# Optimization experiments

Measured on AMD Instinct MI355X. Metric: run time of the kernel, lower is better.

The kernel has to match this reference:

```python
import jax, jax.numpy as jnp
import numpy as np

FILTER_LENGTH = 2048
HOP_LENGTH = 512
CUTOFF = FILTER_LENGTH // 2 + 1  # 1025


def _make_forward_basis():
    # Real/imag rows of DFT matrix, modulated by periodic Hann window.
    fourier_basis = np.fft.fft(np.eye(FILTER_LENGTH))
    basis = np.vstack([np.real(fourier_basis[:CUTOFF, :]),
                       np.imag(fourier_basis[:CUTOFF, :])])  # [2050, 2048]
    n = np.arange(FILTER_LENGTH)
    hann = 0.5 - 0.5 * np.cos(2.0 * np.pi * n / FILTER_LENGTH)  # fftbins=True
    basis = basis * hann[None, :]
    return jnp.asarray(basis[:, None, :], dtype=jnp.float32)  # [2050, 1, 2048]


def setup_inputs() -> dict:
    key = jax.random.key(0)
    input_data = jax.random.normal(key, (32, 320000), dtype=jnp.float32)
    forward_basis = _make_forward_basis()
    return {"input_data": input_data, "forward_basis": forward_basis}


def reference(input_data, forward_basis):
    B = input_data.shape[0]
    pad = FILTER_LENGTH // 2
    x = jnp.pad(input_data, ((0, 0), (pad, pad)), mode="reflect")  # [B, N+2048]
    x = x[:, None, :]  # [B, 1, T]
    ft = jax.lax.conv_general_dilated(
        x, forward_basis,
        window_strides=(HOP_LENGTH,),
        padding="VALID",
        dimension_numbers=("NCH", "OIH", "NCH"),
    )  # [B, 2050, frames]
    real = ft[:, :CUTOFF, :]
    imag = ft[:, CUTOFF:, :]
    return jnp.sqrt(real * real + imag * imag)
```

## Files before the change

kernel.cpp:

```cpp
#include <hip/hip_runtime.h>
#include <hip/hip_bf16.h>
#include <cstdint>


#define FILT   2048
#define HOP    512
#define CUT    1025
#define NBATCH 32
#define TFR    626
#define NFR    (NBATCH * TFR)
#define LSIG   320000
#define LPAD   (LSIG + FILT)
#define N2     1024
#define MWS    1088
#define KT     17
#define TT     20

typedef __attribute__((ext_vector_type(8))) short short8;

__device__ __forceinline__ short bf16r(float f) {
  __hip_bfloat16 h = __float2bfloat16(f);
  return __builtin_bit_cast(short, h);
}
__device__ __forceinline__ float bf2f(uint32_t u) {
  return __builtin_bit_cast(float, u << 16);
}

__device__ __forceinline__ short8 pack8(float4 a, float4 b) {
  short8 v;
  v[0] = bf16r(a.x); v[1] = bf16r(a.y); v[2] = bf16r(a.z); v[3] = bf16r(a.w);
  v[4] = bf16r(b.x); v[5] = bf16r(b.y); v[6] = bf16r(b.z); v[7] = bf16r(b.w);
  return v;
}

__global__ void pad_signal(const float* __restrict__ x, short* __restrict__ XP) {
  const int b = blockIdx.y;
  const int i0 = (blockIdx.x * 256 + threadIdx.x) * 8;
  if (i0 >= LPAD) return;
  const float* xb = x + (size_t)b * LSIG;
  const int j0 = i0 - 1024;
  short8 v;
  if (j0 >= 0 && j0 + 8 <= LSIG) {
    float4 a = *(const float4*)(xb + j0);
    float4 c = *(const float4*)(xb + j0 + 4);
    v = pack8(a, c);
  } else {
    #pragma unroll
    for (int e = 0; e < 8; ++e) {
      int j = j0 + e;
      j = j < 0 ? -j : (j >= LSIG ? 2 * LSIG - 2 - j : j);
      v[e] = bf16r(xb[j]);
    }
  }
  *(short8*)&XP[(size_t)b * LPAD + i0] = v;
}

__global__ void make_tables(float* __restrict__ hann, float2* __restrict__ Tst,
                            float2* __restrict__ Tun) {
  const int i = blockIdx.x * 256 + threadIdx.x;
  const float PI2 = 6.283185307179586f;
  if (i < 2048) hann[i] = 0.5f - 0.5f * cosf(PI2 * (float)i / 2048.0f);
  if (i < 1024) {
    float s, c;
    sincosf(-PI2 * (float)i / 1024.0f, &s, &c);
    Tst[i] = make_float2(c, s);
    sincosf(-PI2 * (float)i / 2048.0f, &s, &c);
    Tun[i] = make_float2(c, s);
  }
}

__device__ __forceinline__ float2 cmul(float2 a, float2 b) {
  return make_float2(a.x * b.x - a.y * b.y, a.x * b.y + a.y * b.x);
}
__device__ __forceinline__ float2 cmulc(float2 a, float cx, float cy) {
  return make_float2(a.x * cx - a.y * cy, a.x * cy + a.y * cx);
}

__device__ __forceinline__ int SW(int i) { return i ^ ((i >> 4) & 15); }

__device__ __forceinline__ void fft16(float2* y) {
  static constexpr float TX[4][4] = {
    {1.f, 1.f, 1.f, 1.f},
    {1.f,  0.92387953251128674f,  0.70710678118654752f,  0.38268343236508978f},
    {1.f,  0.70710678118654752f,  0.f,                  -0.70710678118654752f},
    {1.f,  0.38268343236508978f, -0.70710678118654752f, -0.92387953251128674f}};
  static constexpr float TY[4][4] = {
    {0.f, 0.f, 0.f, 0.f},
    {0.f, -0.38268343236508978f, -0.70710678118654752f, -0.92387953251128674f},
    {0.f, -0.70710678118654752f, -1.f,                  -0.70710678118654752f},
    {0.f, -0.92387953251128674f, -0.70710678118654752f,  0.38268343236508978f}};
  float2 G[16];
  #pragma unroll
  for (int n0 = 0; n0 < 4; ++n0) {
    float2 a0 = y[n0], a1 = y[n0 + 4], a2 = y[n0 + 8], a3 = y[n0 + 12];
    float2 e = make_float2(a0.x + a2.x, a0.y + a2.y);
    float2 f = make_float2(a0.x - a2.x, a0.y - a2.y);
    float2 g = make_float2(a1.x + a3.x, a1.y + a3.y);
    float2 h = make_float2(a1.x - a3.x, a1.y - a3.y);
    float2 F0 = make_float2(e.x + g.x, e.y + g.y);
    float2 F1 = make_float2(f.x + h.y, f.y - h.x);
    float2 F2 = make_float2(e.x - g.x, e.y - g.y);
    float2 F3 = make_float2(f.x - h.y, f.y + h.x);
    G[n0 * 4 + 0] = F0;
    G[n0 * 4 + 1] = cmulc(F1, TX[n0][1], TY[n0][1]);
    G[n0 * 4 + 2] = cmulc(F2, TX[n0][2], TY[n0][2]);
    G[n0 * 4 + 3] = cmulc(F3, TX[n0][3], TY[n0][3]);
  }
  #pragma unroll
  for (int q = 0; q < 4; ++q) {
    float2 a0 = G[q], a1 = G[4 + q], a2 = G[8 + q], a3 = G[12 + q];
    float2 e = make_float2(a0.x + a2.x, a0.y + a2.y);
    float2 f = make_float2(a0.x - a2.x, a0.y - a2.y);
    float2 g = make_float2(a1.x + a3.x, a1.y + a3.y);
    float2 h = make_float2(a1.x - a3.x, a1.y - a3.y);
    y[q]      = make_float2(e.x + g.x, e.y + g.y);
    y[q + 4]  = make_float2(f.x + h.y, f.y - h.x);
    y[q + 8]  = make_float2(e.x - g.x, e.y - g.y);
    y[q + 12] = make_float2(f.x - h.y, f.y + h.x);
  }
}

template<int LOG>
__device__ __forceinline__ void fft_stage(float2* z, const float2* tw, int lane) {
  constexpr int M4 = 1 << LOG;
  constexpr int STRIDE = 1 << (8 - LOG);
  #pragma unroll
  for (int u = 0; u < 4; ++u) {
    const int bf = u * 64 + lane;
    const int j  = bf & (M4 - 1);
    const int i0 = ((bf >> LOG) << (LOG + 2)) | j;
    const int i1 = i0 + M4, i2 = i0 + 2 * M4, i3 = i0 + 3 * M4;
    const int p0 = SW(i0), p1 = SW(i1), p2 = SW(i2), p3 = SW(i3);
    float2 a = z[p0], b = z[p1], c = z[p2], d = z[p3];
    if (LOG > 0) {
      b = cmul(b, tw[j * STRIDE]);
      c = cmul(c, tw[2 * j * STRIDE]);
      d = cmul(d, tw[3 * j * STRIDE]);
    }
    const float2 t0 = make_float2(a.x + c.x, a.y + c.y);
    const float2 t1 = make_float2(a.x - c.x, a.y - c.y);
    const float2 t2 = make_float2(b.x + d.x, b.y + d.y);
    const float2 t3 = make_float2(b.x - d.x, b.y - d.y);
    z[p0] = make_float2(t0.x + t2.x, t0.y + t2.y);
    z[p1] = make_float2(t1.x + t3.y, t1.y - t3.x);
    z[p2] = make_float2(t0.x - t2.x, t0.y - t2.y);
    z[p3] = make_float2(t1.x - t3.y, t1.y + t3.x);
  }
}

__global__ __launch_bounds__(256)
void stft_fft(const short* __restrict__ XP, const float* __restrict__ hann,
              const float2* __restrict__ Tst, const float2* __restrict__ Tun,
              ushort* __restrict__ MW)
{
  __shared__ float2 zsh[4][1024];
  __shared__ float2 tst[1024];

  const int tid = threadIdx.x, wv = tid >> 6, lane = tid & 63;
  #pragma unroll
  for (int u = 0; u < 4; ++u) tst[u * 256 + tid] = Tst[u * 256 + tid];
  __syncthreads();

  float2* z = zsh[wv];

  const int G  = ((lane & 3) << 4) | (lane & 12) | (lane >> 4);
  const int zb = 16 * G, gm = G & 15;

  const int f = blockIdx.x * 4 + wv;
  const int b = f / TFR, t = f - b * TFR;
  const short* base = XP + (size_t)b * LPAD + (size_t)t * HOP;

  float2 y[16];
  #pragma unroll
  for (int u = 0; u < 16; ++u) {
    const int n = u * 64 + lane;
    const uint32_t pr = *(const uint32_t*)(base + 2 * n);
    const float2 h = *(const float2*)(hann + 2 * n);
    y[u] = make_float2(bf2f(pr & 0xffffu) * h.x, bf2f(pr >> 16) * h.y);
  }
  fft16(y);
  #pragma unroll
  for (int k = 0; k < 16; ++k) z[zb + (k ^ gm)] = y[k];

  fft_stage<4>(z, tst, lane);
  fft_stage<6>(z, tst, lane);
  fft_stage<8>(z, tst, lane);

  ushort* mw = MW + (size_t)f * MWS;
  #pragma unroll
  for (int v = 0; v < 8; ++v) {
    const int k = v * 64 + lane;
    const float2 Zk = z[SW(k)];
    const int km = (N2 - k) & (N2 - 1);
    const float2 Zm = z[SW(km)];
    const float xer = 0.5f * (Zk.x + Zm.x);
    const float xei = 0.5f * (Zk.y - Zm.y);
    const float xor_ = 0.5f * (Zk.y + Zm.y);
    const float xoi = -0.5f * (Zk.x - Zm.x);
    const float2 w = Tun[k];
    const float px = w.x * xor_ - w.y * xoi;
    const float py = w.x * xoi + w.y * xor_;
    const float Xr = xer + px, Xi = xei + py;
    const float Yr = xer - px, Yi = xei - py;
    mw[k]        = (ushort)bf16r(sqrtf(Xr * Xr + Xi * Xi));
    mw[1024 - k] = (ushort)bf16r(sqrtf(Yr * Yr + Yi * Yi));
  }
  if (lane == 0) {
    const float2 Zc = z[SW(512)];
    mw[512] = (ushort)bf16r(sqrtf(Zc.x * Zc.x + Zc.y * Zc.y));
  }
}

__global__ __launch_bounds__(256)
void transpose_out(const ushort* __restrict__ MW, float* __restrict__ out) {
  __shared__ float tile[64][33];
  const int b  = blockIdx.y;
  const int kt = blockIdx.x % KT;
  const int tt = blockIdx.x / KT;
  const int k0 = kt * 64, t0 = tt * 32;
  const int tid = threadIdx.x;
  const int r = tid >> 5, c = tid & 31;

  #pragma unroll
  for (int s = 0; s < 4; ++s) {
    const int t = t0 + r + 8 * s;
    if (t < TFR) {
      const uint32_t pr =
        *(const uint32_t*)(MW + (size_t)(b * TFR + t) * MWS + k0 + 2 * c);
      tile[2 * c][r + 8 * s]     = bf2f(pr & 0xffffu);
      tile[2 * c + 1][r + 8 * s] = bf2f(pr >> 16);
    }
  }
  __syncthreads();

  const int kk = tid >> 2, toff = (tid & 3) * 8;
  const int k = k0 + kk;
  if (k < CUT) {
    float* pptr = out + (size_t)b * (CUT * TFR) + (size_t)k * TFR + t0 + toff;
    if (t0 + 32 <= TFR) {
      float4 v0 = make_float4(tile[kk][toff], tile[kk][toff + 1],
                              tile[kk][toff + 2], tile[kk][toff + 3]);
      float4 v1 = make_float4(tile[kk][toff + 4], tile[kk][toff + 5],
                              tile[kk][toff + 6], tile[kk][toff + 7]);
      *(float4*)pptr = v0;
      *(float4*)(pptr + 4) = v1;
    } else {
      #pragma unroll
      for (int e = 0; e < 8; ++e) {
        const int t = t0 + toff + e;
        if (t < TFR) pptr[e] = tile[kk][toff + e];
      }
    }
  }
}

typedef __attribute__((ext_vector_type(4))) float f32x4;

__global__ __launch_bounds__(256, 2)
void stft_gemm_fb(const float* __restrict__ basis, const float* __restrict__ x,
                  float* __restrict__ out)
{
  __shared__ alignas(16) short sA[2][128][64];
  __shared__ alignas(16) short sB[128][64];

  const int tid  = threadIdx.x;
  const int wave = tid >> 6;
  const int lane = tid & 63;
  const int n0 = blockIdx.x * 128;
  const int m0 = blockIdx.y * 128;

  f32x4 acc_r[4][4], acc_i[4][4];
  #pragma unroll
  for (int i = 0; i < 4; ++i)
    #pragma unroll
    for (int j = 0; j < 4; ++j) { acc_r[i][j] = (f32x4)0.f; acc_i[i][j] = (f32x4)0.f; }

  const int sr = tid >> 1;
  const int sh = (tid & 1) * 32;

  for (int k0 = 0; k0 < FILT; k0 += 64) {
    #pragma unroll
    for (int p = 0; p < 2; ++p) {
      const int k = m0 + sr;
      short8 v[4];
      if (k < CUT) {
        const float* src = basis + (size_t)(p * CUT + k) * FILT + k0 + sh;
        #pragma unroll
        for (int qq = 0; qq < 4; ++qq) {
          float4 a = *(const float4*)(src + qq * 8);
          float4 b = *(const float4*)(src + qq * 8 + 4);
          v[qq] = pack8(a, b);
        }
      } else {
        #pragma unroll
        for (int qq = 0; qq < 4; ++qq) v[qq] = (short8)(short)0;
      }
      #pragma unroll
      for (int qq = 0; qq < 4; ++qq) *(short8*)&sA[p][sr][sh + qq * 8] = v[qq];
    }
    {
      const int f = n0 + sr;
      short8 v[4];
      if (f < NFR) {
        const int b = f / TFR, t = f - b * TFR;
        const float* xb = x + (size_t)b * LSIG;
        const int j0 = t * HOP + k0 + sh - 1024;
        if (j0 >= 0 && j0 + 32 <= LSIG) {
          #pragma unroll
          for (int qq = 0; qq < 4; ++qq) {
            float4 a  = *(const float4*)(xb + j0 + qq * 8);
            float4 b2 = *(const float4*)(xb + j0 + qq * 8 + 4);
            v[qq] = pack8(a, b2);
          }
        } else {
          #pragma unroll
          for (int qq = 0; qq < 4; ++qq)
            #pragma unroll
            for (int e = 0; e < 8; ++e) {
              int j = j0 + qq * 8 + e;
              j = j < 0 ? -j : (j >= LSIG ? 2 * LSIG - 2 - j : j);
              v[qq][e] = bf16r(xb[j]);
            }
        }
      } else {
        #pragma unroll
        for (int qq = 0; qq < 4; ++qq) v[qq] = (short8)(short)0;
      }
      #pragma unroll
      for (int qq = 0; qq < 4; ++qq) *(short8*)&sB[sr][sh + qq * 8] = v[qq];
    }
    __syncthreads();

    const int ra = lane & 15;
    #pragma unroll
    for (int kk = 0; kk < 64; kk += 32) {
      const int col = kk + (lane >> 4) * 8;
      short8 arr[4], aii[4], bfr[4];
      #pragma unroll
      for (int i = 0; i < 4; ++i) {
        const int rm = (wave >> 1) * 64 + i * 16 + ra;
        arr[i] = *(const short8*)&sA[0][rm][col];
        aii[i] = *(const short8*)&sA[1][rm][col];
        const int rn = (wave & 1) * 64 + i * 16 + ra;
        bfr[i] = *(const short8*)&sB[rn][col];
      }
      #pragma unroll
      for (int i = 0; i < 4; ++i)
        #pragma unroll
        for (int j = 0; j < 4; ++j) {
          acc_r[i][j] = __builtin_amdgcn_mfma_f32_16x16x32_bf16(arr[i], bfr[j], acc_r[i][j], 0, 0, 0);
          acc_i[i][j] = __builtin_amdgcn_mfma_f32_16x16x32_bf16(aii[i], bfr[j], acc_i[i][j], 0, 0, 0);
        }
    }
    __syncthreads();
  }

  const int wm0 = m0 + (wave >> 1) * 64;
  const int wn0 = n0 + (wave & 1) * 64;
  const int cl = lane & 15;
  const int rg = (lane >> 4) * 4;
  #pragma unroll
  for (int j = 0; j < 4; ++j) {
    const int f = wn0 + j * 16 + cl;
    if (f >= NFR) continue;
    const int b = f / TFR, t = f - b * TFR;
    float* ob = out + (size_t)b * (CUT * TFR) + t;
    #pragma unroll
    for (int i = 0; i < 4; ++i) {
      #pragma unroll
      for (int r = 0; r < 4; ++r) {
        const int k = wm0 + i * 16 + rg + r;
        if (k < CUT) {
          float re = acc_r[i][j][r], im = acc_i[i][j][r];
          ob[(size_t)k * TFR] = sqrtf(re * re + im * im);
        }
      }
    }
  }
}

extern "C" void kernel_launch(void* const* d_in, const int* in_sizes, int n_in,
                              void* d_out, int out_size, void* d_ws, size_t ws_size,
                              hipStream_t stream) {
  const float* x     = (const float*)d_in[0];
  const float* basis = (const float*)d_in[1];
  float* out = (float*)d_out;

  const size_t sbytes = (size_t)NBATCH * LPAD * sizeof(short);
  const size_t hbytes = 2048 * sizeof(float);
  const size_t tbytes = 1024 * sizeof(float2);
  const size_t mbytes = (size_t)NFR * MWS * sizeof(ushort);

  if (ws_size >= sbytes + hbytes + 2 * tbytes + mbytes) {
    short*  XP   = (short*)d_ws;
    float*  hann = (float*)((char*)d_ws + sbytes);
    float2* Tst  = (float2*)((char*)d_ws + sbytes + hbytes);
    float2* Tun  = (float2*)((char*)d_ws + sbytes + hbytes + tbytes);
    ushort* MW   = (ushort*)((char*)d_ws + sbytes + hbytes + 2 * tbytes);
    pad_signal<<<dim3((LPAD + 2047) / 2048, NBATCH), 256, 0, stream>>>(x, XP);
    make_tables<<<8, 256, 0, stream>>>(hann, Tst, Tun);
    stft_fft<<<NFR / 4, 256, 0, stream>>>(XP, hann, Tst, Tun, MW);
    transpose_out<<<dim3(KT * TT, NBATCH), 256, 0, stream>>>(MW, out);
  } else {
    stft_gemm_fb<<<dim3(157, 9), 256, 0, stream>>>(basis, x, out);
  }
}
```

Baseline: 96.39 us.

## Fuse reflect padding into FFT kernel and merge two radix-4 stages in registers

Removes the separate pad_signal kernel that wrote a bf16 padded copy of the signal; the FFT kernel now reads fp32 input directly, handling reflect padding only for edge frames. It also merges the first two shared-memory radix-4 stages into a single register-resident radix-16 pass, cutting one round of LDS writes and reads. This saves a kernel launch and an intermediate buffer round trip, at the cost of doubled input read bytes per frame (fp32 instead of bf16) and more registers.

```diff
diff --git a/kernel.cpp b/kernel.cpp
--- a/kernel.cpp
+++ b/kernel.cpp
@@ -10,7 +10,6 @@
 #define TFR    626
 #define NFR    (NBATCH * TFR)
 #define LSIG   320000
-#define LPAD   (LSIG + FILT)
 #define N2     1024
 #define MWS    1088
 #define KT     17
@@ -31,28 +30,6 @@
   v[0] = bf16r(a.x); v[1] = bf16r(a.y); v[2] = bf16r(a.z); v[3] = bf16r(a.w);
   v[4] = bf16r(b.x); v[5] = bf16r(b.y); v[6] = bf16r(b.z); v[7] = bf16r(b.w);
   return v;
-}
-
-__global__ void pad_signal(const float* __restrict__ x, short* __restrict__ XP) {
-  const int b = blockIdx.y;
-  const int i0 = (blockIdx.x * 256 + threadIdx.x) * 8;
-  if (i0 >= LPAD) return;
-  const float* xb = x + (size_t)b * LSIG;
-  const int j0 = i0 - 1024;
-  short8 v;
-  if (j0 >= 0 && j0 + 8 <= LSIG) {
-    float4 a = *(const float4*)(xb + j0);
-    float4 c = *(const float4*)(xb + j0 + 4);
-    v = pack8(a, c);
-  } else {
-    #pragma unroll
-    for (int e = 0; e < 8; ++e) {
-      int j = j0 + e;
-      j = j < 0 ? -j : (j >= LSIG ? 2 * LSIG - 2 - j : j);
-      v[e] = bf16r(xb[j]);
-    }
-  }
-  *(short8*)&XP[(size_t)b * LPAD + i0] = v;
 }
 
 __global__ void make_tables(float* __restrict__ hann, float2* __restrict__ Tst,
@@ -149,7 +126,7 @@
 }
 
 __global__ __launch_bounds__(256)
-void stft_fft(const short* __restrict__ XP, const float* __restrict__ hann,
+void stft_fft(const float* __restrict__ x, const float* __restrict__ hann,
               const float2* __restrict__ Tst, const float2* __restrict__ Tun,
               ushort* __restrict__ MW)
 {
@@ -165,25 +142,83 @@
 
   const int G  = ((lane & 3) << 4) | (lane & 12) | (lane >> 4);
   const int zb = 16 * G, gm = G & 15;
+  const int j0 = lane & 15, B = lane >> 4;
 
   const int f = blockIdx.x * 4 + wv;
   const int b = f / TFR, t = f - b * TFR;
-  const short* base = XP + (size_t)b * LPAD + (size_t)t * HOP;
+  const float* xb = x + (size_t)b * LSIG;
+  const int off = t * HOP - 1024;
 
   float2 y[16];
-  #pragma unroll
-  for (int u = 0; u < 16; ++u) {
-    const int n = u * 64 + lane;
-    const uint32_t pr = *(const uint32_t*)(base + 2 * n);
-    const float2 h = *(const float2*)(hann + 2 * n);
-    y[u] = make_float2(bf2f(pr & 0xffffu) * h.x, bf2f(pr >> 16) * h.y);
+  if (t >= 2 && t <= 623) {
+    #pragma unroll
+    for (int u = 0; u < 16; ++u) {
+      const int n = u * 64 + lane;
+      const float2 p = *(const float2*)(xb + off + 2 * n);
+      const float2 h = *(const float2*)(hann + 2 * n);
+      y[u] = make_float2(p.x * h.x, p.y * h.y);
+    }
+  } else {
+    #pragma unroll
+    for (int u = 0; u < 16; ++u) {
+      const int n = u * 64 + lane;
+      int ja = off + 2 * n, jb = ja + 1;
+      ja = ja < 0 ? -ja : (ja >= LSIG ? 2 * LSIG - 2 - ja : ja);
+      jb = jb < 0 ? -jb : (jb >= LSIG ? 2 * LSIG - 2 - jb : jb);
+      const float2 h = *(const float2*)(hann + 2 * n);
+      y[u] = make_float2(xb[ja] * h.x, xb[jb] * h.y);
+    }
   }
   fft16(y);
   #pragma unroll
   for (int k = 0; k < 16; ++k) z[zb + (k ^ gm)] = y[k];
 
-  fft_stage<4>(z, tst, lane);
-  fft_stage<6>(z, tst, lane);
+  {
+    float2 g[4][4];
+    #pragma unroll
+    for (int a = 0; a < 4; ++a)
+      #pragma unroll
+      for (int b2 = 0; b2 < 4; ++b2)
+        g[a][b2] = z[16 * (a + 4 * b2 + 16 * B) + (j0 ^ (a + 4 * b2))];
+    const float2 w41 = tst[16 * j0], w42 = tst[32 * j0], w43 = tst[48 * j0];
+    #pragma unroll
+    for (int b2 = 0; b2 < 4; ++b2) {
+      float2 a0 = g[0][b2];
+      float2 a1 = cmul(g[1][b2], w41);
+      float2 a2 = cmul(g[2][b2], w42);
+      float2 a3 = cmul(g[3][b2], w43);
+      const float2 t0 = make_float2(a0.x + a2.x, a0.y + a2.y);
+      const float2 t1 = make_float2(a0.x - a2.x, a0.y - a2.y);
+      const float2 t2 = make_float2(a1.x + a3.x, a1.y + a3.y);
+      const float2 t3 = make_float2(a1.x - a3.x, a1.y - a3.y);
+      g[0][b2] = make_float2(t0.x + t2.x, t0.y + t2.y);
+      g[1][b2] = make_float2(t1.x + t3.y, t1.y - t3.x);
+      g[2][b2] = make_float2(t0.x - t2.x, t0.y - t2.y);
+      g[3][b2] = make_float2(t1.x - t3.y, t1.y + t3.x);
+    }
+    #pragma unroll
+    for (int mp = 0; mp < 4; ++mp) {
+      const int jj = 4 * (j0 + 16 * mp);
+      float2 a0 = g[mp][0];
+      float2 a1 = cmul(g[mp][1], tst[jj]);
+      float2 a2 = cmul(g[mp][2], tst[2 * jj]);
+      float2 a3 = cmul(g[mp][3], tst[3 * jj]);
+      const float2 t0 = make_float2(a0.x + a2.x, a0.y + a2.y);
+      const float2 t1 = make_float2(a0.x - a2.x, a0.y - a2.y);
+      const float2 t2 = make_float2(a1.x + a3.x, a1.y + a3.y);
+      const float2 t3 = make_float2(a1.x - a3.x, a1.y - a3.y);
+      g[mp][0] = make_float2(t0.x + t2.x, t0.y + t2.y);
+      g[mp][1] = make_float2(t1.x + t3.y, t1.y - t3.x);
+      g[mp][2] = make_float2(t0.x - t2.x, t0.y - t2.y);
+      g[mp][3] = make_float2(t1.x - t3.y, t1.y + t3.x);
+    }
+    #pragma unroll
+    for (int mp = 0; mp < 4; ++mp)
+      #pragma unroll
+      for (int m2 = 0; m2 < 4; ++m2)
+        z[16 * (mp + 4 * m2 + 16 * B) + (j0 ^ (mp + 4 * m2))] = g[mp][m2];
+  }
+
   fft_stage<8>(z, tst, lane);
 
   ushort* mw = MW + (size_t)f * MWS;
@@ -386,20 +421,17 @@
   const float* basis = (const float*)d_in[1];
   float* out = (float*)d_out;
 
-  const size_t sbytes = (size_t)NBATCH * LPAD * sizeof(short);
   const size_t hbytes = 2048 * sizeof(float);
   const size_t tbytes = 1024 * sizeof(float2);
   const size_t mbytes = (size_t)NFR * MWS * sizeof(ushort);
 
-  if (ws_size >= sbytes + hbytes + 2 * tbytes + mbytes) {
-    short*  XP   = (short*)d_ws;
-    float*  hann = (float*)((char*)d_ws + sbytes);
-    float2* Tst  = (float2*)((char*)d_ws + sbytes + hbytes);
-    float2* Tun  = (float2*)((char*)d_ws + sbytes + hbytes + tbytes);
-    ushort* MW   = (ushort*)((char*)d_ws + sbytes + hbytes + 2 * tbytes);
-    pad_signal<<<dim3((LPAD + 2047) / 2048, NBATCH), 256, 0, stream>>>(x, XP);
+  if (ws_size >= hbytes + 2 * tbytes + mbytes) {
+    float*  hann = (float*)d_ws;
+    float2* Tst  = (float2*)((char*)d_ws + hbytes);
+    float2* Tun  = (float2*)((char*)d_ws + hbytes + tbytes);
+    ushort* MW   = (ushort*)((char*)d_ws + hbytes + 2 * tbytes);
     make_tables<<<8, 256, 0, stream>>>(hann, Tst, Tun);
-    stft_fft<<<NFR / 4, 256, 0, stream>>>(XP, hann, Tst, Tun, MW);
+    stft_fft<<<NFR / 4, 256, 0, stream>>>(x, hann, Tst, Tun, MW);
     transpose_out<<<dim3(KT * TT, NBATCH), 256, 0, stream>>>(MW, out);
   } else {
     stft_gemm_fb<<<dim3(157, 9), 256, 0, stream>>>(basis, x, out);
```

Measured after the change: 89.04 us, median of 2. 1.08x faster.
